# Kernel optimization log

Hardware: AMD Instinct MI355X
Metric: run time of the kernel (lower is better)

Reference implementation:

```python
import jax, jax.numpy as jnp
import numpy as np

EPS = 1e-5
QMAX = 127.0


def fake_quant_int8(x):
    """Per-tensor symmetric int8 fake-quant (quantize+dequantize), dynamic scale.
    Mirrors brevitas Int8ActPerTensorFloat / Int8WeightPerTensorFloat math."""
    scale = jnp.maximum(jnp.max(jnp.abs(x)) / QMAX, 1e-8)
    q = jnp.clip(jnp.round(x / scale), -128.0, 127.0) * scale
    # straight-through estimator (identity grad through quant)
    return x + jax.lax.stop_gradient(q - x)


def layer_norm(x, g, b):
    mu = jnp.mean(x, axis=-1, keepdims=True)
    var = jnp.mean(jnp.square(x - mu), axis=-1, keepdims=True)
    return (x - mu) * jax.lax.rsqrt(var + EPS) * g + b


def setup_inputs() -> dict:
    key = jax.random.key(0)
    B, S, D, H = 64, 196, 768, 12
    M = 4 * D
    ks = jax.random.split(key, 8)
    s = lambda d: 1.0 / np.sqrt(d)
    return {
        "x": jax.random.normal(ks[0], (B, S, D), jnp.float32),
        "ln1_g": jnp.ones((D,), jnp.float32),
        "ln1_b": jnp.zeros((D,), jnp.float32),
        "ln2_g": jnp.ones((D,), jnp.float32),
        "ln2_b": jnp.zeros((D,), jnp.float32),
        "w_qkv": jax.random.normal(ks[1], (D, 3 * D), jnp.float32) * s(D),
        "b_qkv": jnp.zeros((3 * D,), jnp.float32),
        "w_o": jax.random.normal(ks[2], (D, D), jnp.float32) * s(D),
        "b_o": jnp.zeros((D,), jnp.float32),
        "w1": jax.random.normal(ks[3], (D, M), jnp.float32) * s(D),
        "b1": jnp.zeros((M,), jnp.float32),
        "w2": jax.random.normal(ks[4], (M, D), jnp.float32) * s(M),
        "b2": jnp.zeros((D,), jnp.float32),
    }


def _block(x, ln1_g, ln1_b, ln2_g, ln2_b, w_qkv, b_qkv, w_o, b_o, w1, b1, w2, b2):
    B, S, D = x.shape
    H = 12
    hd = D // H

    # --- LN -> quant -> MHSA -> add ---
    r1 = x
    h = fake_quant_int8(layer_norm(x, ln1_g, ln1_b))
    qkv = jnp.einsum("bsd,de->bse", h, fake_quant_int8(w_qkv)) + b_qkv
    q, k, v = jnp.split(qkv, 3, axis=-1)
    q = q.reshape(B, S, H, hd)
    k = k.reshape(B, S, H, hd)
    v = v.reshape(B, S, H, hd)
    logits = jnp.einsum("bqhd,bkhd->bhqk", q, k) / jnp.sqrt(jnp.float32(hd))
    attn = jax.nn.softmax(logits, axis=-1)
    ctx = jnp.einsum("bhqk,bkhd->bqhd", attn, v).reshape(B, S, D)
    ctx = fake_quant_int8(ctx)
    mhsa = jnp.einsum("bsd,de->bse", ctx, fake_quant_int8(w_o)) + b_o
    x = mhsa + r1

    # --- LN -> quant -> MLP (fc1 -> GELU -> quant -> fc2) -> add ---
    r2 = x
    h = fake_quant_int8(layer_norm(x, ln2_g, ln2_b))
    h = jnp.einsum("bsd,dm->bsm", h, fake_quant_int8(w1)) + b1
    h = jax.nn.gelu(h, approximate=False)  # torch nn.GELU default = exact erf
    h = fake_quant_int8(h)
    h = jnp.einsum("bsm,md->bsd", h, fake_quant_int8(w2)) + b2
    return h + r2


def reference(x, ln1_g, ln1_b, ln2_g, ln2_b, w_qkv, b_qkv, w_o, b_o, w1, b1, w2, b2):
    return _block(x, ln1_g, ln1_b, ln2_g, ln2_b, w_qkv, b_qkv, w_o, b_o, w1, b1, w2, b2)
```

## Files before the change

### kernel.cpp

```cpp
#include <hip/hip_runtime.h>
#include <cstdint>
#include <cstddef>

#define DEVFN __device__ __forceinline__

typedef short bf16x8 __attribute__((ext_vector_type(8)));
typedef float f32x4  __attribute__((ext_vector_type(4)));
typedef int   i32x4  __attribute__((ext_vector_type(4)));

static constexpr int NTOK  = 64 * 196;
static constexpr int DMODEL= 768;
static constexpr int NHEAD = 12;
static constexpr int NQKV  = 2304;
static constexpr int MMLP  = 3072;
static constexpr int SEQ   = 196;
static constexpr int NBATCH= 64;

enum { SL_LN1=0, SL_WQKV=1, SL_CTX=2, SL_WO=3, SL_LN2=4, SL_W1=5, SL_GELU=6, SL_W2=7 };

static constexpr int NSH       = 64;
static constexpr int SH_STRIDE = 64;
static constexpr int SLOTS_U32 = NSH * SH_STRIDE;

DEVFN float bf2f(unsigned short u){ return __uint_as_float(((unsigned)u) << 16); }
DEVFN unsigned short f2bf(float f){
  unsigned u = __float_as_uint(f);
  u += 0x7fffu + ((u >> 16) & 1u);
  return (unsigned short)(u >> 16);
}
DEVFN void split_bf(float v, unsigned short& hi, unsigned short& lo){
  hi = f2bf(v);
  lo = f2bf(v - bf2f(hi));
}
DEVFN float slot_absmax(const unsigned* __restrict__ slots, int slot){
  unsigned m = 0u;
#pragma unroll
  for (int j = 0; j < NSH; j++){
    unsigned u = slots[j * SH_STRIDE + slot];
    m = (u > m) ? u : m;
  }
  return __uint_as_float(m);
}
DEVFN float slot_scale(const unsigned* __restrict__ slots, int slot){
  return fmaxf(slot_absmax(slots, slot) / 127.0f, 1e-8f);
}
DEVFN void scatter_amax(unsigned* slots, int slot, unsigned bucket, float v){
  atomicMax(slots + (bucket & (NSH - 1)) * SH_STRIDE + slot, __float_as_uint(v));
}
DEVFN float quantval(float x, float s){
  float q = rintf(x / s);
  return fminf(fmaxf(q, -128.0f), 127.0f);
}
DEVFN unsigned pack4(float a, float b, float c, float d){
  return  ((unsigned)(unsigned char)(char)(int)a)
        | ((unsigned)(unsigned char)(char)(int)b << 8)
        | ((unsigned)(unsigned char)(char)(int)c << 16)
        | ((unsigned)(unsigned char)(char)(int)d << 24);
}
DEVFN float gelu_fast(float v){
  float s  = v * 0.70710678118654752f;
  float ax = fabsf(s);
  float t  = __builtin_amdgcn_rcpf(fmaf(0.3275911f, ax, 1.0f));
  float p  = t * fmaf(t, fmaf(t, fmaf(t, fmaf(t, 1.061405429f, -1.453152027f),
                                      1.421413741f), -0.284496736f), 0.254829592f);
  float er = fmaf(-p, __expf(-ax * ax), 1.0f);
  unsigned sgn = __float_as_uint(s) & 0x80000000u;
  er = __uint_as_float(__float_as_uint(er) | sgn);
  return 0.5f * v * (1.0f + er);
}
DEVFN f32x4 mfma16(bf16x8 a, bf16x8 b, f32x4 c){
  return __builtin_amdgcn_mfma_f32_16x16x32_bf16(a, b, c, 0, 0, 0);
}
DEVFN i32x4 mfma16i8(i32x4 a, i32x4 b, i32x4 c){
  return __builtin_amdgcn_mfma_i32_16x16x64_i8(a, b, c, 0, 0, 0);
}
DEVFN void async_ld16(const void* g, void* lds){
  __builtin_amdgcn_global_load_lds((const __attribute__((address_space(1))) void*)g,
                                   (__attribute__((address_space(3))) void*)lds, 16, 0, 0);
}

__global__ void k_init(unsigned* slots){
  int i = blockIdx.x * blockDim.x + threadIdx.x;
  if (i < SLOTS_U32) slots[i] = 0u;
}

__global__ void k_absmax(const float* __restrict__ x, int n4, unsigned* slots, int slot){
  float m = 0.f;
  const float4* x4 = (const float4*)x;
  int stride = gridDim.x * blockDim.x;
  for (int j = blockIdx.x * blockDim.x + threadIdx.x; j < n4; j += stride){
    float4 v = x4[j];
    m = fmaxf(m, fmaxf(fmaxf(fabsf(v.x), fabsf(v.y)), fmaxf(fabsf(v.z), fabsf(v.w))));
  }
  for (int off = 32; off; off >>= 1) m = fmaxf(m, __shfl_xor(m, off));
  __shared__ float wm[4];
  int lane = threadIdx.x & 63, w = threadIdx.x >> 6;
  if (lane == 0) wm[w] = m;
  __syncthreads();
  if (threadIdx.x == 0){
    float bm = fmaxf(fmaxf(wm[0], wm[1]), fmaxf(wm[2], wm[3]));
    scatter_amax(slots, slot, blockIdx.x, bm);
  }
}

__global__ void k_quant_transpose(const float* __restrict__ w, char* __restrict__ wt,
                                  int K, int N, const unsigned* __restrict__ slots, int slot){
  __shared__ float tile[32][33];
  float s = slot_scale(slots, slot);
  int n0 = blockIdx.x * 32, k0 = blockIdx.y * 32;
  int tx = threadIdx.x & 31, ty = threadIdx.x >> 5;
#pragma unroll
  for (int i = 0; i < 4; i++){
    int k = k0 + ty + i * 8;
    float v = w[(size_t)k * N + n0 + tx];
    tile[ty + i * 8][tx] = quantval(v, s);
  }
  __syncthreads();
  int n = threadIdx.x >> 3, kg = threadIdx.x & 7;
  unsigned o = pack4(tile[kg * 4 + 0][n], tile[kg * 4 + 1][n],
                     tile[kg * 4 + 2][n], tile[kg * 4 + 3][n]);
  *(unsigned*)(wt + (size_t)(n0 + n) * K + k0 + kg * 4) = o;
}

__global__ void k_layernorm(const float* __restrict__ x, const float* __restrict__ g,
                            const float* __restrict__ b, float* __restrict__ out,
                            unsigned* slots, int slot){
  int w = threadIdx.x >> 6, lane = threadIdx.x & 63;
  int row = blockIdx.x * 4 + w;
  const float4* xr = (const float4*)(x + (size_t)row * DMODEL);
  float4 v[3];
  float sum = 0.f;
#pragma unroll
  for (int i = 0; i < 3; i++){ v[i] = xr[i * 64 + lane]; sum += v[i].x + v[i].y + v[i].z + v[i].w; }
  for (int off = 32; off; off >>= 1) sum += __shfl_xor(sum, off);
  float mu = sum * (1.0f / 768.0f);
  float vs = 0.f;
#pragma unroll
  for (int i = 0; i < 3; i++){
    float dx = v[i].x - mu, dy = v[i].y - mu, dz = v[i].z - mu, dw = v[i].w - mu;
    vs += dx * dx + dy * dy + dz * dz + dw * dw;
  }
  for (int off = 32; off; off >>= 1) vs += __shfl_xor(vs, off);
  float inv = 1.0f / sqrtf(vs * (1.0f / 768.0f) + 1e-5f);
  const float4* g4 = (const float4*)g; const float4* b4 = (const float4*)b;
  float4* o4 = (float4*)(out + (size_t)row * DMODEL);
  float am = 0.f;
#pragma unroll
  for (int i = 0; i < 3; i++){
    float4 gg = g4[i * 64 + lane], bb = b4[i * 64 + lane], o;
    o.x = (v[i].x - mu) * inv * gg.x + bb.x;
    o.y = (v[i].y - mu) * inv * gg.y + bb.y;
    o.z = (v[i].z - mu) * inv * gg.z + bb.z;
    o.w = (v[i].w - mu) * inv * gg.w + bb.w;
    am = fmaxf(am, fmaxf(fmaxf(fabsf(o.x), fabsf(o.y)), fmaxf(fabsf(o.z), fabsf(o.w))));
    o4[i * 64 + lane] = o;
  }
  for (int off = 32; off; off >>= 1) am = fmaxf(am, __shfl_xor(am, off));
  __shared__ float am4[4];
  if (lane == 0) am4[w] = am;
  __syncthreads();
  if (threadIdx.x == 0){
    float bm = fmaxf(fmaxf(am4[0], am4[1]), fmaxf(am4[2], am4[3]));
    scatter_amax(slots, slot, blockIdx.x, bm);
  }
}

__global__ void k_quant_act(const float* __restrict__ x, unsigned* __restrict__ out,
                            int n4, const unsigned* __restrict__ slots, int slot){
  float s = slot_scale(slots, slot);
  const float4* x4 = (const float4*)x;
  int stride = gridDim.x * blockDim.x;
  for (int j = blockIdx.x * blockDim.x + threadIdx.x; j < n4; j += stride){
    float4 v = x4[j];
    out[j] = pack4(quantval(v.x, s), quantval(v.y, s), quantval(v.z, s), quantval(v.w, s));
  }
}

__global__ void k_quant_bf16_i8(const unsigned short* __restrict__ x, unsigned* __restrict__ out,
                                int n4, const unsigned* __restrict__ slots, int slot){
  float s = slot_scale(slots, slot);
  const ushort4* x4 = (const ushort4*)x;
  int stride = gridDim.x * blockDim.x;
  for (int j = blockIdx.x * blockDim.x + threadIdx.x; j < n4; j += stride){
    ushort4 v = x4[j];
    out[j] = pack4(quantval(bf2f(v.x), s), quantval(bf2f(v.y), s),
                   quantval(bf2f(v.z), s), quantval(bf2f(v.w), s));
  }
}

template<int EPI>
__launch_bounds__(256, 4)
__global__ void k_gemm(const char* __restrict__ A,
                       const char* __restrict__ Bt,
                       const float* __restrict__ bias,
                       const float* __restrict__ res,
                       float* __restrict__ Cf,
                       unsigned short* __restrict__ Cb,
                       const unsigned* __restrict__ slots, int sa_slot, int sb_slot,
                       unsigned* gmax_slots, int gmax_slot,
                       int M, int N, int K)
{
  __shared__ __align__(16) char smem[32768];
  __shared__ float gm4[4];
  const int tid  = threadIdx.x;
  const int lane = tid & 63;
  const int wv   = tid >> 6;
  const int wx   = wv & 1, wy = wv >> 1;
  const int quad = lane >> 4;
  const int l16  = lane & 15;
  const int m0 = blockIdx.y * 128, n0 = blockIdx.x * 128;

  auto issue = [&](int k0, int buf){
#pragma unroll
    for (int i = 0; i < 2; i++){
      int c = tid + i * 256;
      int row = c >> 2, q = c & 3;
      int qs = (q - ((row + (row >> 2)) & 3)) & 3;
      async_ld16(A + (size_t)(m0 + row) * K + k0 + qs * 16,
                 smem + buf * 8192 + (i * 256 + wv * 64) * 16);
    }
#pragma unroll
    for (int i = 0; i < 2; i++){
      int c = tid + i * 256;
      int row = c >> 2, q = c & 3;
      int qs = (q - ((row + (row >> 2)) & 3)) & 3;
      async_ld16(Bt + (size_t)(n0 + row) * K + k0 + qs * 16,
                 smem + 16384 + buf * 8192 + (i * 256 + wv * 64) * 16);
    }
  };

  i32x4 acc[4][4] = {};
  const int nk = K >> 6;
  issue(0, 0);

  const int ch = (((quad + (l16 & 3) + (l16 >> 2)) & 3)) * 16;

  for (int k = 0; k < nk; k++){
    const int cur = k & 1;
    if (k + 1 < nk){
      issue((k + 1) << 6, cur ^ 1);
      asm volatile("s_waitcnt vmcnt(4)" ::: "memory");
    } else {
      asm volatile("s_waitcnt vmcnt(0)" ::: "memory");
    }
    asm volatile("s_barrier" ::: "memory");

    const char* Ab = smem + cur * 8192;
    const char* Bb = smem + 16384 + cur * 8192;
    i32x4 af[4], bfr[4];
#pragma unroll
    for (int i = 0; i < 4; i++)
      af[i] = *(const i32x4*)(Ab + (wy * 64 + i * 16 + l16) * 64 + ch);
#pragma unroll
    for (int j = 0; j < 4; j++)
      bfr[j] = *(const i32x4*)(Bb + (wx * 64 + j * 16 + l16) * 64 + ch);
    asm volatile("s_waitcnt lgkmcnt(0)" ::: "memory");
    asm volatile("s_barrier" ::: "memory");

#pragma unroll
    for (int i = 0; i < 4; i++)
#pragma unroll
      for (int j = 0; j < 4; j++)
        acc[i][j] = mfma16i8(af[i], bfr[j], acc[i][j]);
  }
  __syncthreads();

  float (*stage)[132] = (float (*)[132])smem;
  const float sc = slot_scale(slots, sa_slot) * slot_scale(slots, sb_slot);
  const int col4 = (tid & 31) * 4;
  const int gc   = n0 + col4;
  const float4 bb = *(const float4*)&bias[gc];
  float gmax = 0.f;
#pragma unroll
  for (int i = 0; i < 4; i++){
#pragma unroll
    for (int j = 0; j < 4; j++)
#pragma unroll
      for (int r = 0; r < 4; r++)
        stage[wy * 16 + quad * 4 + r][wx * 64 + j * 16 + l16] = (float)acc[i][j][r];
    __syncthreads();
#pragma unroll
    for (int rr = 0; rr < 4; rr++){
      const int rl = rr * 8 + (tid >> 5);
      const int gm = m0 + ((rl >> 4) * 64) + i * 16 + (rl & 15);
      float4 v = *(const float4*)&stage[rl][col4];
      v.x = v.x * sc + bb.x; v.y = v.y * sc + bb.y;
      v.z = v.z * sc + bb.z; v.w = v.w * sc + bb.w;
      if constexpr (EPI == 1){
        float4 rv = *(const float4*)&res[(size_t)gm * N + gc];
        v.x += rv.x; v.y += rv.y; v.z += rv.z; v.w += rv.w;
        *(float4*)&Cf[(size_t)gm * N + gc] = v;
      } else if constexpr (EPI == 2){
        float g0 = gelu_fast(v.x);
        float g1 = gelu_fast(v.y);
        float g2 = gelu_fast(v.z);
        float g3 = gelu_fast(v.w);
        gmax = fmaxf(gmax, fmaxf(fmaxf(fabsf(g0), fabsf(g1)), fmaxf(fabsf(g2), fabsf(g3))));
        ushort4 o = {f2bf(g0), f2bf(g1), f2bf(g2), f2bf(g3)};
        *(ushort4*)&Cb[(size_t)gm * N + gc] = o;
      } else {
        *(float4*)&Cf[(size_t)gm * N + gc] = v;
      }
    }
    __syncthreads();
  }
  if constexpr (EPI == 2){
    for (int off = 32; off; off >>= 1) gmax = fmaxf(gmax, __shfl_xor(gmax, off));
    if (lane == 0) gm4[wv] = gmax;
    __syncthreads();
    if (tid == 0){
      float bm = fmaxf(fmaxf(gm4[0], gm4[1]), fmaxf(gm4[2], gm4[3]));
      scatter_amax(gmax_slots, gmax_slot, blockIdx.x + blockIdx.y * gridDim.x, bm);
    }
  }
}

__launch_bounds__(512, 2)
__global__ void k_attention(const float* __restrict__ qkv, float* __restrict__ ctx,
                            unsigned* slots){
  __shared__ __align__(16) unsigned short Khi[208 * 72], Klo[208 * 72];
  __shared__ __align__(16) unsigned short Vhi[64 * 232], Vlo[64 * 232];
  __shared__ __align__(16) unsigned short Ps[8][2][16 * 40];
  __shared__ float gm8[8];

  const int bh = blockIdx.x;
  const int b = bh / NHEAD, h = bh % NHEAD;
  const float* base = qkv + (size_t)b * SEQ * NQKV;
  const int tid = threadIdx.x, lane = tid & 63, wv = tid >> 6;
  const int quad = lane >> 4, l16 = lane & 15;

  for (int idx = tid; idx < 208 * 16; idx += 512){
    int r = idx >> 4, c4 = (idx & 15) * 4;
    float4 v = {0.f, 0.f, 0.f, 0.f};
    if (r < SEQ) v = *(const float4*)(base + (size_t)r * NQKV + DMODEL + h * 64 + c4);
    unsigned short h0,l0,h1,l1,h2,l2,h3,l3;
    split_bf(v.x, h0, l0); split_bf(v.y, h1, l1); split_bf(v.z, h2, l2); split_bf(v.w, h3, l3);
    ushort4 hs = {h0, h1, h2, h3}, ls = {l0, l1, l2, l3};
    *(ushort4*)(Khi + r * 72 + c4) = hs;
    *(ushort4*)(Klo + r * 72 + c4) = ls;
  }
  for (int idx = tid; idx < SEQ * 16; idx += 512){
    int s = idx >> 4, dg = (idx & 15) * 4;
    float4 v = *(const float4*)(base + (size_t)s * NQKV + 2 * DMODEL + h * 64 + dg);
    unsigned short hi, lo;
    split_bf(v.x, hi, lo); Vhi[(dg + 0) * 232 + s] = hi; Vlo[(dg + 0) * 232 + s] = lo;
    split_bf(v.y, hi, lo); Vhi[(dg + 1) * 232 + s] = hi; Vlo[(dg + 1) * 232 + s] = lo;
    split_bf(v.z, hi, lo); Vhi[(dg + 2) * 232 + s] = hi; Vlo[(dg + 2) * 232 + s] = lo;
    split_bf(v.w, hi, lo); Vhi[(dg + 3) * 232 + s] = hi; Vlo[(dg + 3) * 232 + s] = lo;
  }
  for (int idx = tid; idx < 64 * 36; idx += 512){
    int d = idx / 36, c = idx - d * 36;
    Vhi[d * 232 + SEQ + c] = 0; Vlo[d * 232 + SEQ + c] = 0;
  }
  __syncthreads();

  unsigned short* PsH = &Ps[wv][0][0];
  unsigned short* PsL = &Ps[wv][1][0];

  float gmax = 0.f;
  for (int qt = wv; qt < 13; qt += 8){
    const int q0 = qt * 16;
    const int sq = q0 + l16;
    const bool valid = sq < SEQ;

    bf16x8 aqh[2], aql[2];
    const float* qrow = base + (size_t)(valid ? sq : 0) * NQKV + h * 64;
#pragma unroll
    for (int ks = 0; ks < 2; ks++){
      float4 v0 = {0,0,0,0}, v1 = {0,0,0,0};
      if (valid){
        v0 = *(const float4*)(qrow + ks * 32 + quad * 8);
        v1 = *(const float4*)(qrow + ks * 32 + quad * 8 + 4);
      }
      float vv[8] = {v0.x, v0.y, v0.z, v0.w, v1.x, v1.y, v1.z, v1.w};
#pragma unroll
      for (int j = 0; j < 8; j++){
        unsigned short hi, lo; split_bf(vv[j], hi, lo);
        aqh[ks][j] = (short)hi; aql[ks][j] = (short)lo;
      }
    }

    f32x4 sacc[13];
#pragma unroll
    for (int t = 0; t < 13; t++){
      f32x4 a = {0.f, 0.f, 0.f, 0.f};
#pragma unroll
      for (int ks = 0; ks < 2; ks++){
        bf16x8 bkh = *(const bf16x8*)(Khi + (t * 16 + l16) * 72 + ks * 32 + quad * 8);
        bf16x8 bkl = *(const bf16x8*)(Klo + (t * 16 + l16) * 72 + ks * 32 + quad * 8);
        a = mfma16(aqh[ks], bkh, a);
        a = mfma16(aqh[ks], bkl, a);
        a = mfma16(aql[ks], bkh, a);
      }
      sacc[t] = a;
    }

    float mx[4] = {-1e30f, -1e30f, -1e30f, -1e30f};
#pragma unroll
    for (int t = 0; t < 13; t++){
      bool dead = (t == 12) && (l16 >= 4);
#pragma unroll
      for (int r = 0; r < 4; r++){
        float v = dead ? -1e30f : sacc[t][r] * 0.125f;
        sacc[t][r] = v;
        mx[r] = fmaxf(mx[r], v);
      }
    }
#pragma unroll
    for (int off = 1; off < 16; off <<= 1)
#pragma unroll
      for (int r = 0; r < 4; r++) mx[r] = fmaxf(mx[r], __shfl_xor(mx[r], off));
    float sum[4] = {0.f, 0.f, 0.f, 0.f};
#pragma unroll
    for (int t = 0; t < 13; t++)
#pragma unroll
      for (int r = 0; r < 4; r++){
        float e = __expf(sacc[t][r] - mx[r]);
        sacc[t][r] = e; sum[r] += e;
      }
#pragma unroll
    for (int off = 1; off < 16; off <<= 1)
#pragma unroll
      for (int r = 0; r < 4; r++) sum[r] += __shfl_xor(sum[r], off);
    float inv[4];
#pragma unroll
    for (int r = 0; r < 4; r++) inv[r] = 1.0f / sum[r];

    f32x4 oacc[4] = {};
#pragma unroll
    for (int ks = 0; ks < 7; ks++){
      const int t0 = 2 * ks, t1 = 2 * ks + 1;
#pragma unroll
      for (int r = 0; r < 4; r++){
        int row = quad * 4 + r;
        unsigned short hi, lo;
        split_bf(sacc[t0][r] * inv[r], hi, lo);
        PsH[row * 40 + l16] = hi; PsL[row * 40 + l16] = lo;
        if (t1 < 13){
          split_bf(sacc[t1][r] * inv[r], hi, lo);
          PsH[row * 40 + 16 + l16] = hi; PsL[row * 40 + 16 + l16] = lo;
        } else {
          PsH[row * 40 + 16 + l16] = 0; PsL[row * 40 + 16 + l16] = 0;
        }
      }
      __builtin_amdgcn_wave_barrier();
      bf16x8 aph = *(const bf16x8*)(PsH + l16 * 40 + quad * 8);
      bf16x8 apl = *(const bf16x8*)(PsL + l16 * 40 + quad * 8);
#pragma unroll
      for (int n = 0; n < 4; n++){
        bf16x8 bvh = *(const bf16x8*)(Vhi + (n * 16 + l16) * 232 + ks * 32 + quad * 8);
        bf16x8 bvl = *(const bf16x8*)(Vlo + (n * 16 + l16) * 232 + ks * 32 + quad * 8);
        oacc[n] = mfma16(aph, bvh, oacc[n]);
        oacc[n] = mfma16(aph, bvl, oacc[n]);
        oacc[n] = mfma16(apl, bvh, oacc[n]);
      }
      __builtin_amdgcn_wave_barrier();
    }

#pragma unroll
    for (int r = 0; r < 4; r++){
      int srow = q0 + quad * 4 + r;
      if (srow < SEQ){
#pragma unroll
        for (int n = 0; n < 4; n++){
          float v = oacc[n][r];
          ctx[((size_t)(b * SEQ + srow)) * DMODEL + h * 64 + n * 16 + l16] = v;
          gmax = fmaxf(gmax, fabsf(v));
        }
      }
    }
  }
  for (int off = 32; off; off >>= 1) gmax = fmaxf(gmax, __shfl_xor(gmax, off));
  if (lane == 0) gm8[wv] = gmax;
  __syncthreads();
  if (tid == 0){
    float bm = 0.f;
#pragma unroll
    for (int i = 0; i < 8; i++) bm = fmaxf(bm, gm8[i]);
    scatter_amax(slots, SL_CTX, blockIdx.x, bm);
  }
}

extern "C" void kernel_launch(void* const* d_in, const int* in_sizes, int n_in,
                              void* d_out, int out_size, void* d_ws, size_t ws_size,
                              hipStream_t stream)
{
  const float* x     = (const float*)d_in[0];
  const float* ln1_g = (const float*)d_in[1];
  const float* ln1_b = (const float*)d_in[2];
  const float* ln2_g = (const float*)d_in[3];
  const float* ln2_b = (const float*)d_in[4];
  const float* w_qkv = (const float*)d_in[5];
  const float* b_qkv = (const float*)d_in[6];
  const float* w_o   = (const float*)d_in[7];
  const float* b_o   = (const float*)d_in[8];
  const float* w1    = (const float*)d_in[9];
  const float* b1    = (const float*)d_in[10];
  const float* w2    = (const float*)d_in[11];
  const float* b2    = (const float*)d_in[12];

  char* ws = (char*)d_ws;
  size_t off = 0;
  unsigned* slots = (unsigned*)ws;                 off += SLOTS_U32 * 4;
  char* wqkvT = (char*)(ws + off); off += (size_t)NQKV  * DMODEL;
  char* woT   = (char*)(ws + off); off += (size_t)DMODEL* DMODEL;
  char* w1T   = (char*)(ws + off); off += (size_t)MMLP  * DMODEL;
  char* w2T   = (char*)(ws + off); off += (size_t)DMODEL* MMLP;
  off = (off + 255) & ~(size_t)255;
  float* t1    = (float*)(ws + off);               off += (size_t)NTOK * DMODEL * 4;
  char*  t1q   = (char*)(ws + off);                off += (size_t)NTOK * DMODEL;
  off = (off + 255) & ~(size_t)255;
  float* qkv   = (float*)(ws + off);               off += (size_t)NTOK * NQKV * 4;
  float* xmid  = (float*)(ws + off);               off += (size_t)NTOK * DMODEL * 4;
  unsigned short* h1 = (unsigned short*)qkv;
  char* h1q = (char*)qkv + (size_t)NTOK * MMLP * 2;
  float* outp = (float*)d_out;

  k_init<<<(SLOTS_U32 + 255) / 256, 256, 0, stream>>>(slots);

  k_absmax<<<256, 256, 0, stream>>>(w_qkv, DMODEL * NQKV / 4, slots, SL_WQKV);
  k_absmax<<<128, 256, 0, stream>>>(w_o,   DMODEL * DMODEL / 4, slots, SL_WO);
  k_absmax<<<256, 256, 0, stream>>>(w1,    DMODEL * MMLP / 4, slots, SL_W1);
  k_absmax<<<256, 256, 0, stream>>>(w2,    MMLP * DMODEL / 4, slots, SL_W2);

  k_quant_transpose<<<dim3(NQKV / 32, DMODEL / 32), 256, 0, stream>>>(w_qkv, wqkvT, DMODEL, NQKV, slots, SL_WQKV);
  k_quant_transpose<<<dim3(DMODEL / 32, DMODEL / 32), 256, 0, stream>>>(w_o, woT, DMODEL, DMODEL, slots, SL_WO);
  k_quant_transpose<<<dim3(MMLP / 32, DMODEL / 32), 256, 0, stream>>>(w1, w1T, DMODEL, MMLP, slots, SL_W1);
  k_quant_transpose<<<dim3(DMODEL / 32, MMLP / 32), 256, 0, stream>>>(w2, w2T, MMLP, DMODEL, slots, SL_W2);

  k_layernorm<<<NTOK / 4, 256, 0, stream>>>(x, ln1_g, ln1_b, t1, slots, SL_LN1);
  {
    int n4 = NTOK * DMODEL / 4;
    k_quant_act<<<(n4 + 255) / 256, 256, 0, stream>>>(t1, (unsigned*)t1q, n4, slots, SL_LN1);
  }
  k_gemm<0><<<dim3(NQKV / 128, NTOK / 128), 256, 0, stream>>>(
      t1q, wqkvT, b_qkv, nullptr, qkv, nullptr, slots, SL_LN1, SL_WQKV, nullptr, 0,
      NTOK, NQKV, DMODEL);

  k_attention<<<NBATCH * NHEAD, 512, 0, stream>>>(qkv, t1, slots);
  {
    int n4 = NTOK * DMODEL / 4;
    k_quant_act<<<(n4 + 255) / 256, 256, 0, stream>>>(t1, (unsigned*)t1q, n4, slots, SL_CTX);
  }
  k_gemm<1><<<dim3(DMODEL / 128, NTOK / 128), 256, 0, stream>>>(
      t1q, woT, b_o, x, xmid, nullptr, slots, SL_CTX, SL_WO, nullptr, 0,
      NTOK, DMODEL, DMODEL);

  k_layernorm<<<NTOK / 4, 256, 0, stream>>>(xmid, ln2_g, ln2_b, t1, slots, SL_LN2);
  {
    int n4 = NTOK * DMODEL / 4;
    k_quant_act<<<(n4 + 255) / 256, 256, 0, stream>>>(t1, (unsigned*)t1q, n4, slots, SL_LN2);
  }
  k_gemm<2><<<dim3(MMLP / 128, NTOK / 128), 256, 0, stream>>>(
      t1q, w1T, b1, nullptr, nullptr, h1, slots, SL_LN2, SL_W1, slots, SL_GELU,
      NTOK, MMLP, DMODEL);
  {
    int n4 = NTOK * MMLP / 4;
    k_quant_bf16_i8<<<(n4 + 255) / 256, 256, 0, stream>>>(h1, (unsigned*)h1q, n4, slots, SL_GELU);
  }
  k_gemm<1><<<dim3(DMODEL / 128, NTOK / 128), 256, 0, stream>>>(
      h1q, w2T, b2, xmid, outp, nullptr, slots, SL_GELU, SL_W2, nullptr, 0,
      NTOK, DMODEL, MMLP);
}
```

Measured before the change: 515.1 us.

## Fuse weight absmax launches and swizzle attention V tile in LDS

The four per-weight absmax kernels become one launch that routes each block range to a weight tensor, cutting launch overhead. In the attention kernel, K and V global loads are first issued into registers and then split and written to LDS, so more loads are in flight at once. V's transposed LDS layout moves from a padded stride to a 256-wide XOR swizzle, meant to cut bank conflicts on the scattered writes and the MFMA operand reads. The cost is higher register pressure from holding 15 float4 values per thread, plus slightly more LDS.

```diff
diff --git a/kernel.cpp b/kernel.cpp
--- a/kernel.cpp
+++ b/kernel.cpp
@@ -78,17 +78,29 @@
   __builtin_amdgcn_global_load_lds((const __attribute__((address_space(1))) void*)g,
                                    (__attribute__((address_space(3))) void*)lds, 16, 0, 0);
 }
+DEVFN int vidx(int d, int s){
+  return d * 256 + (s ^ (((d ^ (d >> 2)) & 7) << 3));
+}
 
 __global__ void k_init(unsigned* slots){
   int i = blockIdx.x * blockDim.x + threadIdx.x;
   if (i < SLOTS_U32) slots[i] = 0u;
 }
 
-__global__ void k_absmax(const float* __restrict__ x, int n4, unsigned* slots, int slot){
+__global__ void k_absmax4(const float* __restrict__ x0, const float* __restrict__ x1,
+                          const float* __restrict__ x2, const float* __restrict__ x3,
+                          unsigned* slots){
+  int bid = blockIdx.x;
+  const float* x; int n4, slot, b0, nb;
+  if (bid < 256)      { x = x0; n4 = DMODEL * NQKV  / 4; slot = SL_WQKV; b0 = 0;   nb = 256; }
+  else if (bid < 384) { x = x1; n4 = DMODEL * DMODEL/ 4; slot = SL_WO;   b0 = 256; nb = 128; }
+  else if (bid < 640) { x = x2; n4 = DMODEL * MMLP  / 4; slot = SL_W1;   b0 = 384; nb = 256; }
+  else                { x = x3; n4 = MMLP   * DMODEL/ 4; slot = SL_W2;   b0 = 640; nb = 256; }
+  int lb = bid - b0;
   float m = 0.f;
   const float4* x4 = (const float4*)x;
-  int stride = gridDim.x * blockDim.x;
-  for (int j = blockIdx.x * blockDim.x + threadIdx.x; j < n4; j += stride){
+  int stride = nb * blockDim.x;
+  for (int j = lb * blockDim.x + threadIdx.x; j < n4; j += stride){
     float4 v = x4[j];
     m = fmaxf(m, fmaxf(fmaxf(fabsf(v.x), fabsf(v.y)), fmaxf(fabsf(v.z), fabsf(v.w))));
   }
@@ -99,7 +111,7 @@
   __syncthreads();
   if (threadIdx.x == 0){
     float bm = fmaxf(fmaxf(wm[0], wm[1]), fmaxf(wm[2], wm[3]));
-    scatter_amax(slots, slot, blockIdx.x, bm);
+    scatter_amax(slots, slot, bid, bm);
   }
 }
 
@@ -319,7 +331,7 @@
 __global__ void k_attention(const float* __restrict__ qkv, float* __restrict__ ctx,
                             unsigned* slots){
   __shared__ __align__(16) unsigned short Khi[208 * 72], Klo[208 * 72];
-  __shared__ __align__(16) unsigned short Vhi[64 * 232], Vlo[64 * 232];
+  __shared__ __align__(16) unsigned short Vhi[64 * 256], Vlo[64 * 256];
   __shared__ __align__(16) unsigned short Ps[8][2][16 * 40];
   __shared__ float gm8[8];
 
@@ -329,28 +341,50 @@
   const int tid = threadIdx.x, lane = tid & 63, wv = tid >> 6;
   const int quad = lane >> 4, l16 = lane & 15;
 
-  for (int idx = tid; idx < 208 * 16; idx += 512){
+  float4 kreg[7], vreg[8];
+#pragma unroll
+  for (int i = 0; i < 7; i++){
+    int idx = tid + i * 512;
     int r = idx >> 4, c4 = (idx & 15) * 4;
     float4 v = {0.f, 0.f, 0.f, 0.f};
-    if (r < SEQ) v = *(const float4*)(base + (size_t)r * NQKV + DMODEL + h * 64 + c4);
-    unsigned short h0,l0,h1,l1,h2,l2,h3,l3;
-    split_bf(v.x, h0, l0); split_bf(v.y, h1, l1); split_bf(v.z, h2, l2); split_bf(v.w, h3, l3);
-    ushort4 hs = {h0, h1, h2, h3}, ls = {l0, l1, l2, l3};
-    *(ushort4*)(Khi + r * 72 + c4) = hs;
-    *(ushort4*)(Klo + r * 72 + c4) = ls;
-  }
-  for (int idx = tid; idx < SEQ * 16; idx += 512){
+    if (idx < 208 * 16 && r < SEQ)
+      v = *(const float4*)(base + (size_t)r * NQKV + DMODEL + h * 64 + c4);
+    kreg[i] = v;
+  }
+#pragma unroll
+  for (int i = 0; i < 8; i++){
+    int idx = tid + i * 512;
     int s = idx >> 4, dg = (idx & 15) * 4;
-    float4 v = *(const float4*)(base + (size_t)s * NQKV + 2 * DMODEL + h * 64 + dg);
-    unsigned short hi, lo;
-    split_bf(v.x, hi, lo); Vhi[(dg + 0) * 232 + s] = hi; Vlo[(dg + 0) * 232 + s] = lo;
-    split_bf(v.y, hi, lo); Vhi[(dg + 1) * 232 + s] = hi; Vlo[(dg + 1) * 232 + s] = lo;
-    split_bf(v.z, hi, lo); Vhi[(dg + 2) * 232 + s] = hi; Vlo[(dg + 2) * 232 + s] = lo;
-    split_bf(v.w, hi, lo); Vhi[(dg + 3) * 232 + s] = hi; Vlo[(dg + 3) * 232 + s] = lo;
-  }
-  for (int idx = tid; idx < 64 * 36; idx += 512){
-    int d = idx / 36, c = idx - d * 36;
-    Vhi[d * 232 + SEQ + c] = 0; Vlo[d * 232 + SEQ + c] = 0;
+    float4 v = {0.f, 0.f, 0.f, 0.f};
+    if (idx < 232 * 16 && s < SEQ)
+      v = *(const float4*)(base + (size_t)s * NQKV + 2 * DMODEL + h * 64 + dg);
+    vreg[i] = v;
+  }
+#pragma unroll
+  for (int i = 0; i < 7; i++){
+    int idx = tid + i * 512;
+    if (idx < 208 * 16){
+      int r = idx >> 4, c4 = (idx & 15) * 4;
+      float4 v = kreg[i];
+      unsigned short h0,l0,h1,l1,h2,l2,h3,l3;
+      split_bf(v.x, h0, l0); split_bf(v.y, h1, l1); split_bf(v.z, h2, l2); split_bf(v.w, h3, l3);
+      ushort4 hs = {h0, h1, h2, h3}, ls = {l0, l1, l2, l3};
+      *(ushort4*)(Khi + r * 72 + c4) = hs;
+      *(ushort4*)(Klo + r * 72 + c4) = ls;
+    }
+  }
+#pragma unroll
+  for (int i = 0; i < 8; i++){
+    int idx = tid + i * 512;
+    if (idx < 232 * 16){
+      int s = idx >> 4, dg = (idx & 15) * 4;
+      float4 v = vreg[i];
+      unsigned short hi, lo;
+      split_bf(v.x, hi, lo); Vhi[vidx(dg + 0, s)] = hi; Vlo[vidx(dg + 0, s)] = lo;
+      split_bf(v.y, hi, lo); Vhi[vidx(dg + 1, s)] = hi; Vlo[vidx(dg + 1, s)] = lo;
+      split_bf(v.z, hi, lo); Vhi[vidx(dg + 2, s)] = hi; Vlo[vidx(dg + 2, s)] = lo;
+      split_bf(v.w, hi, lo); Vhi[vidx(dg + 3, s)] = hi; Vlo[vidx(dg + 3, s)] = lo;
+    }
   }
   __syncthreads();
 
@@ -448,8 +482,8 @@
       bf16x8 apl = *(const bf16x8*)(PsL + l16 * 40 + quad * 8);
 #pragma unroll
       for (int n = 0; n < 4; n++){
-        bf16x8 bvh = *(const bf16x8*)(Vhi + (n * 16 + l16) * 232 + ks * 32 + quad * 8);
-        bf16x8 bvl = *(const bf16x8*)(Vlo + (n * 16 + l16) * 232 + ks * 32 + quad * 8);
+        bf16x8 bvh = *(const bf16x8*)(Vhi + vidx(n * 16 + l16, ks * 32 + quad * 8));
+        bf16x8 bvl = *(const bf16x8*)(Vlo + vidx(n * 16 + l16, ks * 32 + quad * 8));
         oacc[n] = mfma16(aph, bvh, oacc[n]);
         oacc[n] = mfma16(aph, bvl, oacc[n]);
         oacc[n] = mfma16(apl, bvh, oacc[n]);
@@ -518,10 +552,7 @@
 
   k_init<<<(SLOTS_U32 + 255) / 256, 256, 0, stream>>>(slots);
 
-  k_absmax<<<256, 256, 0, stream>>>(w_qkv, DMODEL * NQKV / 4, slots, SL_WQKV);
-  k_absmax<<<128, 256, 0, stream>>>(w_o,   DMODEL * DMODEL / 4, slots, SL_WO);
-  k_absmax<<<256, 256, 0, stream>>>(w1,    DMODEL * MMLP / 4, slots, SL_W1);
-  k_absmax<<<256, 256, 0, stream>>>(w2,    MMLP * DMODEL / 4, slots, SL_W2);
+  k_absmax4<<<896, 256, 0, stream>>>(w_qkv, w_o, w1, w2, slots);
 
   k_quant_transpose<<<dim3(NQKV / 32, DMODEL / 32), 256, 0, stream>>>(w_qkv, wqkvT, DMODEL, NQKV, slots, SL_WQKV);
   k_quant_transpose<<<dim3(DMODEL / 32, DMODEL / 32), 256, 0, stream>>>(w_o, woT, DMODEL, DMODEL, slots, SL_WO);
```

New measurement: 500.9 us. 2.8% less time.
